# Performance work log

Hardware: AMD Instinct MI355X
Metric: run time of the kernel (lower is better)

Reference implementation:

```python
import jax, jax.numpy as jnp
import numpy as np

CZ = 128
MULT = 128
EPS = 1e-5


def _layer_norm(x, w, b):
    mu = jnp.mean(x, axis=-1, keepdims=True)
    var = jnp.mean(jnp.square(x - mu), axis=-1, keepdims=True)
    return (x - mu) * jax.lax.rsqrt(var + EPS) * w + b


def setup_inputs() -> dict:
    key = jax.random.key(0)
    ks = jax.random.split(key, 12)
    N, S, R, Z = 1, 512, 512, CZ
    scale_p = 1.0 / np.sqrt(CZ)
    scale_o = 1.0 / np.sqrt(MULT)
    return {
        "pair_repr": jax.random.normal(ks[0], (N, S, R, Z), jnp.float32),
        "ln_w": jnp.ones((CZ,), jnp.float32),
        "ln_b": jnp.zeros((CZ,), jnp.float32),
        "left1": jax.random.normal(ks[1], (CZ, MULT), jnp.float32) * scale_p,
        "left2": jax.random.normal(ks[2], (CZ, MULT), jnp.float32) * scale_p,
        "right1": jax.random.normal(ks[3], (CZ, MULT), jnp.float32) * scale_p,
        "right2": jax.random.normal(ks[4], (CZ, MULT), jnp.float32) * scale_p,
        "norm_w": jnp.ones((MULT,), jnp.float32),
        "norm_b": jnp.zeros((MULT,), jnp.float32),
        "out_w": jax.random.normal(ks[5], (MULT, CZ), jnp.float32) * scale_o,
        "gate_w": jax.random.normal(ks[6], (CZ, CZ), jnp.float32) * scale_p,
    }


def reference(pair_repr, ln_w, ln_b, left1, left2, right1, right2,
              norm_w, norm_b, out_w, gate_w):
    # pair_repr: [N, S, R, Z]
    residual = pair_repr
    x = _layer_norm(pair_repr, ln_w, ln_b)
    # gated projections (tmu_projection)
    left = jax.nn.sigmoid(x @ left1) * (x @ left2)    # [N,S,R,E]
    right = jax.nn.sigmoid(x @ right1) * (x @ right2)  # [N,T,R,E] (T==S)
    gate = jax.nn.sigmoid(x @ gate_w)                   # [N,S,T,Z]
    # outgoing triangle update (tmo): contract over R
    p = jnp.einsum('nsre,ntre->nste', left, right)      # [N,S,T,E]
    p = _layer_norm(p, norm_w, norm_b)
    p = p @ out_w                                       # [N,S,T,Z]
    p = p * gate
    return residual + p
```

## Files before the change

kernel.cpp:

```cpp
#include <hip/hip_runtime.h>
#include <hip/hip_bf16.h>
#include <stdint.h>

#define ZD 128
#define SD 512
#define MROWS (SD*SD)

typedef __attribute__((ext_vector_type(8))) short short8;
typedef __attribute__((ext_vector_type(4))) float floatx4;
typedef __attribute__((ext_vector_type(4))) unsigned short ushort4v;

__device__ __forceinline__ unsigned short f2bf(float f) {
  union { float f; unsigned u; } c; c.f = f;
  unsigned r = c.u + 0x7FFFu + ((c.u >> 16) & 1u);
  return (unsigned short)(r >> 16);
}
__device__ __forceinline__ float bf2f(unsigned short h) {
  union { unsigned u; float f; } c; c.u = (unsigned)h << 16;
  return c.f;
}
__device__ __forceinline__ float sigm(float x) { return 1.0f / (1.0f + __expf(-x)); }

#define SWZ(r, cb) (((r) << 8) + ((cb) ^ (((r) & 7) << 4)))

__global__ __launch_bounds__(256) void prep_weights(
    const float* __restrict__ l1, const float* __restrict__ l2,
    const float* __restrict__ r1, const float* __restrict__ r2,
    const float* __restrict__ gw, const float* __restrict__ ow,
    unsigned short* __restrict__ dst) {
  const float* srcs[6] = {l1, l2, r1, r2, gw, ow};
  const float* s = srcs[blockIdx.x];
  unsigned short* d = dst + (size_t)blockIdx.x * ZD * ZD;
  for (int i = threadIdx.x; i < ZD * ZD; i += blockDim.x) {
    int k = i >> 7, n = i & 127;
    d[n * ZD + k] = f2bf(s[i]);
  }
}

__global__ __launch_bounds__(256) void ln_kernel(
    const float* __restrict__ in, const float* __restrict__ w,
    const float* __restrict__ b, unsigned short* __restrict__ xo) {
  const int tid = threadIdx.x;
  const int lane = tid & 63;
  const int row = blockIdx.x * 4 + (tid >> 6);
  float2 v = reinterpret_cast<const float2*>(in)[(size_t)row * 64 + lane];
  float s = v.x + v.y, q = v.x * v.x + v.y * v.y;
  #pragma unroll
  for (int m = 1; m < 64; m <<= 1) { s += __shfl_xor(s, m); q += __shfl_xor(q, m); }
  float mu = s * (1.0f / ZD);
  float var = q * (1.0f / ZD) - mu * mu;
  float rstd = rsqrtf(var + 1e-5f);
  float2 wv = reinterpret_cast<const float2*>(w)[lane];
  float2 bv = reinterpret_cast<const float2*>(b)[lane];
  unsigned o0 = f2bf((v.x - mu) * rstd * wv.x + bv.x);
  unsigned o1 = f2bf((v.y - mu) * rstd * wv.y + bv.y);
  reinterpret_cast<unsigned*>(xo)[(size_t)row * 64 + lane] = o0 | (o1 << 16);
}

__global__ __launch_bounds__(256) void proj_kernel(
    const unsigned short* __restrict__ x,
    const unsigned short* __restrict__ wT,
    unsigned short* __restrict__ leftT,
    unsigned short* __restrict__ rightT,
    unsigned short* __restrict__ gateT) {
  __shared__ char xs[32 * 1024];
  __shared__ char w1s[32 * 1024];
  __shared__ char w2s[32 * 1024];
  const int tid = threadIdx.x;
  const int job = blockIdx.y;
  const int m0 = blockIdx.x * 128;

  #pragma unroll
  for (int i = 0; i < 8; ++i) {
    int c = i * 256 + tid;
    int r = c >> 4, cb = (c & 15) << 4;
    *reinterpret_cast<short8*>(xs + SWZ(r, cb)) =
      *reinterpret_cast<const short8*>(x + (size_t)(m0 + r) * ZD + (cb >> 1));
  }
  const unsigned short* wsrc = wT + (size_t)(job == 0 ? 0 : job == 1 ? 2 : 4) * ZD * ZD;
  #pragma unroll
  for (int i = 0; i < 8; ++i) {
    int c = i * 256 + tid;
    int r = c >> 4, cb = (c & 15) << 4;
    *reinterpret_cast<short8*>(w1s + SWZ(r, cb)) =
      *reinterpret_cast<const short8*>(wsrc + r * ZD + (cb >> 1));
  }
  if (job < 2) {
    const unsigned short* w2p = wsrc + ZD * ZD;
    #pragma unroll
    for (int i = 0; i < 8; ++i) {
      int c = i * 256 + tid;
      int r = c >> 4, cb = (c & 15) << 4;
      *reinterpret_cast<short8*>(w2s + SWZ(r, cb)) =
        *reinterpret_cast<const short8*>(w2p + r * ZD + (cb >> 1));
    }
  }
  __syncthreads();

  const int wid = tid >> 6, lane = tid & 63;
  const int msub = (wid >> 1) * 64, esub = (wid & 1) * 64;
  const int fr = lane & 15, fq = lane >> 4;
  const bool two = (job < 2);
  floatx4 acc1[4][4] = {};
  floatx4 acc2[4][4] = {};
  #pragma unroll
  for (int ks = 0; ks < 4; ++ks) {
    const int kb = ks * 64 + fq * 16;
    short8 a[4], b1[4], b2[4];
    #pragma unroll
    for (int i = 0; i < 4; ++i)
      a[i] = *reinterpret_cast<const short8*>(xs + SWZ(msub + i * 16 + fr, kb));
    #pragma unroll
    for (int j = 0; j < 4; ++j) {
      b1[j] = *reinterpret_cast<const short8*>(w1s + SWZ(esub + j * 16 + fr, kb));
      b2[j] = two ? *reinterpret_cast<const short8*>(w2s + SWZ(esub + j * 16 + fr, kb)) : b1[j];
    }
    #pragma unroll
    for (int i = 0; i < 4; ++i)
      #pragma unroll
      for (int j = 0; j < 4; ++j) {
        acc1[i][j] = __builtin_amdgcn_mfma_f32_16x16x32_bf16(a[i], b1[j], acc1[i][j], 0, 0, 0);
        if (two)
          acc2[i][j] = __builtin_amdgcn_mfma_f32_16x16x32_bf16(a[i], b2[j], acc2[i][j], 0, 0, 0);
      }
  }
  unsigned short* dst = (job == 0) ? leftT : (job == 1) ? rightT : gateT;
  #pragma unroll
  for (int i = 0; i < 4; ++i) {
    const int mrow = m0 + msub + i * 16 + fq * 4;
    #pragma unroll
    for (int j = 0; j < 4; ++j) {
      const int e = esub + j * 16 + fr;
      ushort4v pkt;
      #pragma unroll
      for (int r = 0; r < 4; ++r) {
        float v = two ? sigm(acc1[i][j][r]) * acc2[i][j][r] : sigm(acc1[i][j][r]);
        pkt[r] = f2bf(v);
      }
      *reinterpret_cast<ushort4v*>(dst + (size_t)e * MROWS + mrow) = pkt;
    }
  }
}

__global__ __launch_bounds__(256) void einsum_kernel(
    const unsigned short* __restrict__ leftT,
    const unsigned short* __restrict__ rightT,
    unsigned short* __restrict__ pT) {
  __shared__ char at[32 * 1024];
  __shared__ char bt[32 * 1024];
  const int tid = threadIdx.x;
  const int e = blockIdx.z;
  const int t0 = blockIdx.x * 128, s0 = blockIdx.y * 128;
  const unsigned short* Ag = rightT + (size_t)e * MROWS;
  const unsigned short* Bg = leftT  + (size_t)e * MROWS;
  const int wid = tid >> 6, lane = tid & 63;
  const int tsub = (wid >> 1) * 64, ssub = (wid & 1) * 64;
  const int fr = lane & 15, fq = lane >> 4;
  floatx4 acc[4][4] = {};
  for (int ko = 0; ko < 4; ++ko) {
    __syncthreads();
    #pragma unroll
    for (int i = 0; i < 8; ++i) {
      int c = i * 256 + tid;
      int r = c >> 4, cb = (c & 15) << 4;
      *reinterpret_cast<short8*>(at + SWZ(r, cb)) =
        *reinterpret_cast<const short8*>(Ag + (size_t)(t0 + r) * SD + ko * 128 + (cb >> 1));
      *reinterpret_cast<short8*>(bt + SWZ(r, cb)) =
        *reinterpret_cast<const short8*>(Bg + (size_t)(s0 + r) * SD + ko * 128 + (cb >> 1));
    }
    __syncthreads();
    #pragma unroll
    for (int kk = 0; kk < 4; ++kk) {
      const int kb = kk * 64 + fq * 16;
      short8 a[4], b[4];
      #pragma unroll
      for (int i = 0; i < 4; ++i)
        a[i] = *reinterpret_cast<const short8*>(at + SWZ(tsub + i * 16 + fr, kb));
      #pragma unroll
      for (int j = 0; j < 4; ++j)
        b[j] = *reinterpret_cast<const short8*>(bt + SWZ(ssub + j * 16 + fr, kb));
      #pragma unroll
      for (int i = 0; i < 4; ++i)
        #pragma unroll
        for (int j = 0; j < 4; ++j)
          acc[i][j] = __builtin_amdgcn_mfma_f32_16x16x32_bf16(a[i], b[j], acc[i][j], 0, 0, 0);
    }
  }
  unsigned short* Pg = pT + (size_t)e * MROWS;
  #pragma unroll
  for (int i = 0; i < 4; ++i) {
    const int tt = t0 + tsub + i * 16 + fq * 4;
    #pragma unroll
    for (int j = 0; j < 4; ++j) {
      const int ss = s0 + ssub + j * 16 + fr;
      ushort4v pkt;
      #pragma unroll
      for (int r = 0; r < 4; ++r) pkt[r] = f2bf(acc[i][j][r]);
      *reinterpret_cast<ushort4v*>(Pg + (size_t)ss * SD + tt) = pkt;
    }
  }
}

__global__ __launch_bounds__(256) void final_kernel(
    const unsigned short* __restrict__ pT,
    const unsigned short* __restrict__ gateT,
    const unsigned short* __restrict__ owT,
    const float* __restrict__ nw, const float* __restrict__ nb,
    const float* __restrict__ resid, float* __restrict__ out) {
  __shared__ char Pl[128 * 256];
  __shared__ char Pn[128 * 256];
  __shared__ char Gl[128 * 272];
  __shared__ float red[512];
  __shared__ float mu_s[128], rs_s[128], nw_s[128], nb_s[128];
  const int tid = threadIdx.x;
  const int m0 = blockIdx.x * 128;
  #pragma unroll
  for (int i = 0; i < 8; ++i) {
    int c = i * 256 + tid;
    int r = c >> 4, cb = (c & 15) << 4;
    *reinterpret_cast<short8*>(Pl + r * 256 + cb) =
      *reinterpret_cast<const short8*>(pT + (size_t)r * MROWS + m0 + (cb >> 1));
    *reinterpret_cast<short8*>(Gl + r * 272 + cb) =
      *reinterpret_cast<const short8*>(gateT + (size_t)r * MROWS + m0 + (cb >> 1));
  }
  if (tid < 128) { nw_s[tid] = nw[tid]; nb_s[tid] = nb[tid]; }
  __syncthreads();
  const int t = tid & 127, h = tid >> 7;
  const unsigned short* colp = reinterpret_cast<const unsigned short*>(Pl) + t;
  {
    float s = 0.f, q = 0.f;
    for (int e2 = 0; e2 < 64; ++e2) {
      float v = bf2f(colp[(h * 64 + e2) * 128]);
      s += v; q += v * v;
    }
    red[h * 128 + t] = s;
    red[256 + h * 128 + t] = q;
  }
  __syncthreads();
  if (tid < 128) {
    float ss = red[tid] + red[128 + tid];
    float qq = red[256 + tid] + red[384 + tid];
    float mu = ss * (1.f / 128.f);
    float var = qq * (1.f / 128.f) - mu * mu;
    mu_s[tid] = mu;
    rs_s[tid] = rsqrtf(var + 1e-5f);
  }
  __syncthreads();
  {
    float mu = mu_s[t], rs = rs_s[t];
    for (int e2 = 0; e2 < 64; ++e2) {
      int e = h * 64 + e2;
      float v = (bf2f(colp[e * 128]) - mu) * rs * nw_s[e] + nb_s[e];
      *reinterpret_cast<unsigned short*>(Pn + (t << 8) + ((e * 2) ^ ((t & 7) << 4))) = f2bf(v);
    }
  }
  __syncthreads();
  const int wid = tid >> 6, lane = tid & 63;
  const int zsub = (wid >> 1) * 64, tsub = (wid & 1) * 64;
  const int fr = lane & 15, fq = lane >> 4;
  floatx4 acc[4][4] = {};
  #pragma unroll
  for (int ks = 0; ks < 4; ++ks) {
    short8 a[4], b[4];
    #pragma unroll
    for (int i = 0; i < 4; ++i)
      a[i] = *reinterpret_cast<const short8*>(owT + (size_t)(zsub + i * 16 + fr) * ZD + ks * 32 + fq * 8);
    #pragma unroll
    for (int j = 0; j < 4; ++j)
      b[j] = *reinterpret_cast<const short8*>(Pn + SWZ(tsub + j * 16 + fr, ks * 64 + fq * 16));
    #pragma unroll
    for (int i = 0; i < 4; ++i)
      #pragma unroll
      for (int j = 0; j < 4; ++j)
        acc[i][j] = __builtin_amdgcn_mfma_f32_16x16x32_bf16(a[i], b[j], acc[i][j], 0, 0, 0);
  }
  #pragma unroll
  for (int j = 0; j < 4; ++j) {
    const int tt = tsub + j * 16 + fr;
    #pragma unroll
    for (int i = 0; i < 4; ++i) {
      const int zb = zsub + i * 16 + fq * 4;
      const float4 res = *reinterpret_cast<const float4*>(resid + (size_t)(m0 + tt) * ZD + zb);
      float g0 = bf2f(*reinterpret_cast<const unsigned short*>(Gl + (zb + 0) * 272 + tt * 2));
      float g1 = bf2f(*reinterpret_cast<const unsigned short*>(Gl + (zb + 1) * 272 + tt * 2));
      float g2 = bf2f(*reinterpret_cast<const unsigned short*>(Gl + (zb + 2) * 272 + tt * 2));
      float g3 = bf2f(*reinterpret_cast<const unsigned short*>(Gl + (zb + 3) * 272 + tt * 2));
      float4 o;
      o.x = res.x + acc[i][j][0] * g0;
      o.y = res.y + acc[i][j][1] * g1;
      o.z = res.z + acc[i][j][2] * g2;
      o.w = res.w + acc[i][j][3] * g3;
      *reinterpret_cast<float4*>(out + (size_t)(m0 + tt) * ZD + zb) = o;
    }
  }
}

extern "C" void kernel_launch(void* const* d_in, const int* in_sizes, int n_in,
                              void* d_out, int out_size, void* d_ws, size_t ws_size,
                              hipStream_t stream) {
  const float* pair = (const float*)d_in[0];
  const float* ln_w = (const float*)d_in[1];
  const float* ln_b = (const float*)d_in[2];
  const float* l1   = (const float*)d_in[3];
  const float* l2   = (const float*)d_in[4];
  const float* r1   = (const float*)d_in[5];
  const float* r2   = (const float*)d_in[6];
  const float* nw   = (const float*)d_in[7];
  const float* nb   = (const float*)d_in[8];
  const float* ow   = (const float*)d_in[9];
  const float* gw   = (const float*)d_in[10];
  float* out = (float*)d_out;

  unsigned short* xws   = reinterpret_cast<unsigned short*>(d_ws);
  unsigned short* gateT = xws + (size_t)MROWS * ZD;
  unsigned short* wT    = gateT + (size_t)MROWS * ZD;
  unsigned short* owT   = wT + (size_t)5 * ZD * ZD;
  unsigned short* leftT  = reinterpret_cast<unsigned short*>(d_out);
  unsigned short* rightT = leftT + (size_t)MROWS * ZD;
  unsigned short* pTbuf  = xws;

  prep_weights<<<6, 256, 0, stream>>>(l1, l2, r1, r2, gw, ow, wT);
  ln_kernel<<<MROWS / 4, 256, 0, stream>>>(pair, ln_w, ln_b, xws);
  proj_kernel<<<dim3(2048, 3), 256, 0, stream>>>(xws, wT, leftT, rightT, gateT);
  einsum_kernel<<<dim3(4, 4, 128), 256, 0, stream>>>(leftT, rightT, pTbuf);
  final_kernel<<<2048, 256, 0, stream>>>(pTbuf, gateT, owT, nw, nb, pair, out);
}
```

Measured before the change: 604.2 us.

## Merge projection jobs, double-buffer larger einsum tiles, trim final-kernel LDS

The projection kernel now handles all three projections in one block. It loads the activation tile into LDS once and reads the weights straight from global memory instead of staging them in LDS. The einsum kernel grows to 256x256 tiles with 512 threads and a double-buffered 128KB LDS pipeline that prefetches the next K-chunk into registers while computing the current one. The final kernel drops the P staging buffer, reads pT directly from global memory, and switches the gate tile to a swizzled layout. The changes aim to cut redundant x loads, raise einsum data reuse and overlap loads with compute, at the cost of higher register and LDS pressure and lower occupancy.

```diff
diff --git a/kernel.cpp b/kernel.cpp
--- a/kernel.cpp
+++ b/kernel.cpp
@@ -22,6 +22,7 @@
 __device__ __forceinline__ float sigm(float x) { return 1.0f / (1.0f + __expf(-x)); }
 
 #define SWZ(r, cb) (((r) << 8) + ((cb) ^ (((r) & 7) << 4)))
+#define SWZ64(r, cb) (((r) << 7) + ((cb) ^ (((r) & 7) << 4)))
 
 __global__ __launch_bounds__(256) void prep_weights(
     const float* __restrict__ l1, const float* __restrict__ l2,
@@ -57,19 +58,62 @@
   reinterpret_cast<unsigned*>(xo)[(size_t)row * 64 + lane] = o0 | (o1 << 16);
 }
 
+template<bool TWO>
+__device__ __forceinline__ void proj_job(
+    const char* xs, const unsigned short* __restrict__ w1,
+    const unsigned short* __restrict__ w2, unsigned short* __restrict__ dst,
+    int m0, int msub, int esub, int fr, int fq) {
+  floatx4 acc1[4][4] = {};
+  floatx4 acc2[4][4] = {};
+  #pragma unroll
+  for (int ks = 0; ks < 4; ++ks) {
+    const int kb = ks * 64 + fq * 16;
+    const int kw = ks * 32 + fq * 8;
+    short8 a[4], b1[4], b2[4];
+    #pragma unroll
+    for (int i = 0; i < 4; ++i)
+      a[i] = *reinterpret_cast<const short8*>(xs + SWZ(msub + i * 16 + fr, kb));
+    #pragma unroll
+    for (int j = 0; j < 4; ++j) {
+      b1[j] = *reinterpret_cast<const short8*>(w1 + (size_t)(esub + j * 16 + fr) * ZD + kw);
+      if (TWO)
+        b2[j] = *reinterpret_cast<const short8*>(w2 + (size_t)(esub + j * 16 + fr) * ZD + kw);
+    }
+    #pragma unroll
+    for (int i = 0; i < 4; ++i)
+      #pragma unroll
+      for (int j = 0; j < 4; ++j) {
+        acc1[i][j] = __builtin_amdgcn_mfma_f32_16x16x32_bf16(a[i], b1[j], acc1[i][j], 0, 0, 0);
+        if (TWO)
+          acc2[i][j] = __builtin_amdgcn_mfma_f32_16x16x32_bf16(a[i], b2[j], acc2[i][j], 0, 0, 0);
+      }
+  }
+  #pragma unroll
+  for (int i = 0; i < 4; ++i) {
+    const int mrow = m0 + msub + i * 16 + fq * 4;
+    #pragma unroll
+    for (int j = 0; j < 4; ++j) {
+      const int e = esub + j * 16 + fr;
+      ushort4v pkt;
+      #pragma unroll
+      for (int r = 0; r < 4; ++r) {
+        float v = TWO ? sigm(acc1[i][j][r]) * acc2[i][j][r] : sigm(acc1[i][j][r]);
+        pkt[r] = f2bf(v);
+      }
+      *reinterpret_cast<ushort4v*>(dst + (size_t)e * MROWS + mrow) = pkt;
+    }
+  }
+}
+
 __global__ __launch_bounds__(256) void proj_kernel(
     const unsigned short* __restrict__ x,
     const unsigned short* __restrict__ wT,
     unsigned short* __restrict__ leftT,
     unsigned short* __restrict__ rightT,
     unsigned short* __restrict__ gateT) {
-  __shared__ char xs[32 * 1024];
-  __shared__ char w1s[32 * 1024];
-  __shared__ char w2s[32 * 1024];
+  __shared__ char xs[32768];
   const int tid = threadIdx.x;
-  const int job = blockIdx.y;
   const int m0 = blockIdx.x * 128;
-
   #pragma unroll
   for (int i = 0; i < 8; ++i) {
     int c = i * 256 + tid;
@@ -77,118 +121,79 @@
     *reinterpret_cast<short8*>(xs + SWZ(r, cb)) =
       *reinterpret_cast<const short8*>(x + (size_t)(m0 + r) * ZD + (cb >> 1));
   }
-  const unsigned short* wsrc = wT + (size_t)(job == 0 ? 0 : job == 1 ? 2 : 4) * ZD * ZD;
-  #pragma unroll
-  for (int i = 0; i < 8; ++i) {
-    int c = i * 256 + tid;
-    int r = c >> 4, cb = (c & 15) << 4;
-    *reinterpret_cast<short8*>(w1s + SWZ(r, cb)) =
-      *reinterpret_cast<const short8*>(wsrc + r * ZD + (cb >> 1));
-  }
-  if (job < 2) {
-    const unsigned short* w2p = wsrc + ZD * ZD;
-    #pragma unroll
-    for (int i = 0; i < 8; ++i) {
-      int c = i * 256 + tid;
-      int r = c >> 4, cb = (c & 15) << 4;
-      *reinterpret_cast<short8*>(w2s + SWZ(r, cb)) =
-        *reinterpret_cast<const short8*>(w2p + r * ZD + (cb >> 1));
-    }
-  }
   __syncthreads();
-
   const int wid = tid >> 6, lane = tid & 63;
   const int msub = (wid >> 1) * 64, esub = (wid & 1) * 64;
   const int fr = lane & 15, fq = lane >> 4;
-  const bool two = (job < 2);
-  floatx4 acc1[4][4] = {};
-  floatx4 acc2[4][4] = {};
-  #pragma unroll
-  for (int ks = 0; ks < 4; ++ks) {
-    const int kb = ks * 64 + fq * 16;
-    short8 a[4], b1[4], b2[4];
-    #pragma unroll
-    for (int i = 0; i < 4; ++i)
-      a[i] = *reinterpret_cast<const short8*>(xs + SWZ(msub + i * 16 + fr, kb));
-    #pragma unroll
-    for (int j = 0; j < 4; ++j) {
-      b1[j] = *reinterpret_cast<const short8*>(w1s + SWZ(esub + j * 16 + fr, kb));
-      b2[j] = two ? *reinterpret_cast<const short8*>(w2s + SWZ(esub + j * 16 + fr, kb)) : b1[j];
-    }
-    #pragma unroll
-    for (int i = 0; i < 4; ++i)
-      #pragma unroll
-      for (int j = 0; j < 4; ++j) {
-        acc1[i][j] = __builtin_amdgcn_mfma_f32_16x16x32_bf16(a[i], b1[j], acc1[i][j], 0, 0, 0);
-        if (two)
-          acc2[i][j] = __builtin_amdgcn_mfma_f32_16x16x32_bf16(a[i], b2[j], acc2[i][j], 0, 0, 0);
-      }
-  }
-  unsigned short* dst = (job == 0) ? leftT : (job == 1) ? rightT : gateT;
-  #pragma unroll
-  for (int i = 0; i < 4; ++i) {
-    const int mrow = m0 + msub + i * 16 + fq * 4;
-    #pragma unroll
-    for (int j = 0; j < 4; ++j) {
-      const int e = esub + j * 16 + fr;
-      ushort4v pkt;
-      #pragma unroll
-      for (int r = 0; r < 4; ++r) {
-        float v = two ? sigm(acc1[i][j][r]) * acc2[i][j][r] : sigm(acc1[i][j][r]);
-        pkt[r] = f2bf(v);
-      }
-      *reinterpret_cast<ushort4v*>(dst + (size_t)e * MROWS + mrow) = pkt;
-    }
-  }
-}
-
-__global__ __launch_bounds__(256) void einsum_kernel(
+  proj_job<true >(xs, wT,               wT + ZD * ZD,     leftT,  m0, msub, esub, fr, fq);
+  proj_job<true >(xs, wT + 2 * ZD * ZD, wT + 3 * ZD * ZD, rightT, m0, msub, esub, fr, fq);
+  proj_job<false>(xs, wT + 4 * ZD * ZD, nullptr,          gateT,  m0, msub, esub, fr, fq);
+}
+
+__global__ __launch_bounds__(512) void einsum_kernel(
     const unsigned short* __restrict__ leftT,
     const unsigned short* __restrict__ rightT,
     unsigned short* __restrict__ pT) {
-  __shared__ char at[32 * 1024];
-  __shared__ char bt[32 * 1024];
+  __shared__ char lds[131072];
   const int tid = threadIdx.x;
   const int e = blockIdx.z;
-  const int t0 = blockIdx.x * 128, s0 = blockIdx.y * 128;
+  const int t0 = blockIdx.x * 256, s0 = blockIdx.y * 256;
   const unsigned short* Ag = rightT + (size_t)e * MROWS;
   const unsigned short* Bg = leftT  + (size_t)e * MROWS;
   const int wid = tid >> 6, lane = tid & 63;
-  const int tsub = (wid >> 1) * 64, ssub = (wid & 1) * 64;
+  const int tsub = (wid >> 2) * 128, ssub = (wid & 3) * 64;
   const int fr = lane & 15, fq = lane >> 4;
-  floatx4 acc[4][4] = {};
-  for (int ko = 0; ko < 4; ++ko) {
+  floatx4 acc[8][4] = {};
+  short8 stA[4], stB[4];
+
+  const int src_r  = tid >> 3;
+  #define EINS_LOAD(KO)                                                        \
+    _Pragma("unroll")                                                          \
+    for (int i2 = 0; i2 < 4; ++i2) {                                           \
+      int c = i2 * 512 + tid;                                                  \
+      int r = c >> 3, cs = (c & 7) << 3;                                       \
+      stA[i2] = *reinterpret_cast<const short8*>(Ag + (size_t)(t0 + r) * SD + (KO) * 64 + cs); \
+      stB[i2] = *reinterpret_cast<const short8*>(Bg + (size_t)(s0 + r) * SD + (KO) * 64 + cs); \
+    }
+  #define EINS_WRITE(BUF)                                                      \
+    _Pragma("unroll")                                                          \
+    for (int i2 = 0; i2 < 4; ++i2) {                                           \
+      int c = i2 * 512 + tid;                                                  \
+      int r = c >> 3, cb = (c & 7) << 4;                                       \
+      *reinterpret_cast<short8*>(lds + (BUF) * 65536 + SWZ64(r, cb)) = stA[i2];\
+      *reinterpret_cast<short8*>(lds + (BUF) * 65536 + 32768 + SWZ64(r, cb)) = stB[i2]; \
+    }
+
+  EINS_LOAD(0);
+  EINS_WRITE(0);
+  for (int ko = 0; ko < 8; ++ko) {
+    const int cur = ko & 1;
+    if (ko < 7) EINS_LOAD(ko + 1);
     __syncthreads();
-    #pragma unroll
-    for (int i = 0; i < 8; ++i) {
-      int c = i * 256 + tid;
-      int r = c >> 4, cb = (c & 15) << 4;
-      *reinterpret_cast<short8*>(at + SWZ(r, cb)) =
-        *reinterpret_cast<const short8*>(Ag + (size_t)(t0 + r) * SD + ko * 128 + (cb >> 1));
-      *reinterpret_cast<short8*>(bt + SWZ(r, cb)) =
-        *reinterpret_cast<const short8*>(Bg + (size_t)(s0 + r) * SD + ko * 128 + (cb >> 1));
-    }
-    __syncthreads();
-    #pragma unroll
-    for (int kk = 0; kk < 4; ++kk) {
+    const char* Ab = lds + cur * 65536;
+    const char* Bb = Ab + 32768;
+    #pragma unroll
+    for (int kk = 0; kk < 2; ++kk) {
       const int kb = kk * 64 + fq * 16;
-      short8 a[4], b[4];
-      #pragma unroll
-      for (int i = 0; i < 4; ++i)
-        a[i] = *reinterpret_cast<const short8*>(at + SWZ(tsub + i * 16 + fr, kb));
+      short8 a[8], b[4];
+      #pragma unroll
+      for (int i = 0; i < 8; ++i)
+        a[i] = *reinterpret_cast<const short8*>(Ab + SWZ64(tsub + i * 16 + fr, kb));
       #pragma unroll
       for (int j = 0; j < 4; ++j)
-        b[j] = *reinterpret_cast<const short8*>(bt + SWZ(ssub + j * 16 + fr, kb));
-      #pragma unroll
-      for (int i = 0; i < 4; ++i)
+        b[j] = *reinterpret_cast<const short8*>(Bb + SWZ64(ssub + j * 16 + fr, kb));
+      #pragma unroll
+      for (int i = 0; i < 8; ++i)
         #pragma unroll
         for (int j = 0; j < 4; ++j)
           acc[i][j] = __builtin_amdgcn_mfma_f32_16x16x32_bf16(a[i], b[j], acc[i][j], 0, 0, 0);
     }
-  }
+    if (ko < 7) EINS_WRITE(cur ^ 1);
+  }
+  (void)src_r;
   unsigned short* Pg = pT + (size_t)e * MROWS;
   #pragma unroll
-  for (int i = 0; i < 4; ++i) {
+  for (int i = 0; i < 8; ++i) {
     const int tt = t0 + tsub + i * 16 + fq * 4;
     #pragma unroll
     for (int j = 0; j < 4; ++j) {
@@ -207,9 +212,8 @@
     const unsigned short* __restrict__ owT,
     const float* __restrict__ nw, const float* __restrict__ nb,
     const float* __restrict__ resid, float* __restrict__ out) {
-  __shared__ char Pl[128 * 256];
   __shared__ char Pn[128 * 256];
-  __shared__ char Gl[128 * 272];
+  __shared__ char Gl[128 * 256];
   __shared__ float red[512];
   __shared__ float mu_s[128], rs_s[128], nw_s[128], nb_s[128];
   const int tid = threadIdx.x;
@@ -218,19 +222,15 @@
   for (int i = 0; i < 8; ++i) {
     int c = i * 256 + tid;
     int r = c >> 4, cb = (c & 15) << 4;
-    *reinterpret_cast<short8*>(Pl + r * 256 + cb) =
-      *reinterpret_cast<const short8*>(pT + (size_t)r * MROWS + m0 + (cb >> 1));
-    *reinterpret_cast<short8*>(Gl + r * 272 + cb) =
+    *reinterpret_cast<short8*>(Gl + SWZ(r, cb)) =
       *reinterpret_cast<const short8*>(gateT + (size_t)r * MROWS + m0 + (cb >> 1));
   }
   if (tid < 128) { nw_s[tid] = nw[tid]; nb_s[tid] = nb[tid]; }
-  __syncthreads();
   const int t = tid & 127, h = tid >> 7;
-  const unsigned short* colp = reinterpret_cast<const unsigned short*>(Pl) + t;
   {
     float s = 0.f, q = 0.f;
     for (int e2 = 0; e2 < 64; ++e2) {
-      float v = bf2f(colp[(h * 64 + e2) * 128]);
+      float v = bf2f(pT[(size_t)(h * 64 + e2) * MROWS + m0 + t]);
       s += v; q += v * v;
     }
     red[h * 128 + t] = s;
@@ -250,8 +250,8 @@
     float mu = mu_s[t], rs = rs_s[t];
     for (int e2 = 0; e2 < 64; ++e2) {
       int e = h * 64 + e2;
-      float v = (bf2f(colp[e * 128]) - mu) * rs * nw_s[e] + nb_s[e];
-      *reinterpret_cast<unsigned short*>(Pn + (t << 8) + ((e * 2) ^ ((t & 7) << 4))) = f2bf(v);
+      float v = (bf2f(pT[(size_t)e * MROWS + m0 + t]) - mu) * rs * nw_s[e] + nb_s[e];
+      *reinterpret_cast<unsigned short*>(Pn + SWZ(t, e * 2)) = f2bf(v);
     }
   }
   __syncthreads();
@@ -281,10 +281,10 @@
     for (int i = 0; i < 4; ++i) {
       const int zb = zsub + i * 16 + fq * 4;
       const float4 res = *reinterpret_cast<const float4*>(resid + (size_t)(m0 + tt) * ZD + zb);
-      float g0 = bf2f(*reinterpret_cast<const unsigned short*>(Gl + (zb + 0) * 272 + tt * 2));
-      float g1 = bf2f(*reinterpret_cast<const unsigned short*>(Gl + (zb + 1) * 272 + tt * 2));
-      float g2 = bf2f(*reinterpret_cast<const unsigned short*>(Gl + (zb + 2) * 272 + tt * 2));
-      float g3 = bf2f(*reinterpret_cast<const unsigned short*>(Gl + (zb + 3) * 272 + tt * 2));
+      float g0 = bf2f(*reinterpret_cast<const unsigned short*>(Gl + SWZ(zb + 0, tt * 2)));
+      float g1 = bf2f(*reinterpret_cast<const unsigned short*>(Gl + SWZ(zb + 1, tt * 2)));
+      float g2 = bf2f(*reinterpret_cast<const unsigned short*>(Gl + SWZ(zb + 2, tt * 2)));
+      float g3 = bf2f(*reinterpret_cast<const unsigned short*>(Gl + SWZ(zb + 3, tt * 2)));
       float4 o;
       o.x = res.x + acc[i][j][0] * g0;
       o.y = res.y + acc[i][j][1] * g1;
@@ -321,7 +321,7 @@
 
   prep_weights<<<6, 256, 0, stream>>>(l1, l2, r1, r2, gw, ow, wT);
   ln_kernel<<<MROWS / 4, 256, 0, stream>>>(pair, ln_w, ln_b, xws);
-  proj_kernel<<<dim3(2048, 3), 256, 0, stream>>>(xws, wT, leftT, rightT, gateT);
-  einsum_kernel<<<dim3(4, 4, 128), 256, 0, stream>>>(leftT, rightT, pTbuf);
+  proj_kernel<<<2048, 256, 0, stream>>>(xws, wT, leftT, rightT, gateT);
+  einsum_kernel<<<dim3(2, 2, 128), 512, 0, stream>>>(leftT, rightT, pTbuf);
   final_kernel<<<2048, 256, 0, stream>>>(pTbuf, gateT, owT, nw, nb, pair, out);
 }
```

After: 631.5 us. +4.5%, slower.
